# Performance work log

Measured on AMD Instinct MI355X. Metric: run time of the kernel, lower is better.

## Reference

```python
import jax, jax.numpy as jnp
import numpy as np

# Dimensions
F = 512      # features = len(in_degrees)
D = 64
S, B, N = 1, 64, 256   # outer sample dim, hyper-batch, points per batch element
C = 128      # conditioner (phi) feature dim
P = F * F + F  # flat params per batch element: weight + bias


def _mask():
    # hidden-layer MADE degrees: arange(F) % max(1, D-1) + min(1, D-1)
    d = jnp.arange(F) % (D - 1) + 1
    # MaskedLinear hidden mask: out_degrees[:, None] >= in_degrees[None, :]
    # (the torch code reshapes the square [F,F] mask, which is an identity
    #  memory reshape, so element (i, j) = (d[i] >= d[j]))
    return (d[:, None] >= d[None, :]).astype(jnp.float32)


def setup_inputs() -> dict:
    key = jax.random.key(0)
    k1, k2, k3, k4 = jax.random.split(key, 4)
    return {
        "inputs": jax.random.normal(k1, (S, B, N, F), jnp.float32),
        "phi": jax.random.normal(k2, (S, B, C), jnp.float32),
        "Wc": jax.random.normal(k3, (P, C), jnp.float32) * 0.02,
        "bc": jax.random.normal(k4, (P,), jnp.float32) * 0.02,
    }


def reference(inputs, phi, Wc, bc):
    # Conditioner net: linear hypernetwork phi -> flat per-batch params.
    params = jnp.einsum('sbc,pc->sbp', phi, Wc) + bc          # [S,B,P]
    w = params[..., : F * F].reshape(S, B, F, F)               # [S,B,F_in,F_out]
    b = params[..., F * F : F * F + F]                         # [S,B,F]
    mw = w * _mask()                                           # masked per-batch weights

    # Residual block (no batch norm, dropout p=0): act -> masked linear (x2) -> residual
    t = jax.nn.relu(inputs)
    t = jnp.einsum('sbni,sbik->sbnk', t, mw) + b[:, :, None, :]
    t = jax.nn.relu(t)
    # Both MaskedLinear layers split the SAME conditioner output, so they share
    # (w, b); only the masks could differ, and with these degrees they coincide.
    t = jnp.einsum('sbni,sbik->sbnk', t, mw) + b[:, :, None, :]
    return inputs + t
```

## Files before the change

### kernel.cpp

```cpp
#include <hip/hip_runtime.h>
#include <hip/hip_bf16.h>

#define F_   512
#define FF_  (512 * 512)
#define C_   128

typedef __attribute__((ext_vector_type(4))) float f32x4;
typedef __attribute__((ext_vector_type(8))) short s16x8;
typedef __attribute__((ext_vector_type(4))) unsigned short u16x4;

__device__ __forceinline__ unsigned short f2bf(float f) {
    union { __hip_bfloat16 h; unsigned short u; } c;
    c.h = __float2bfloat16(f);
    return c.u;
}

__device__ __forceinline__ s16x8 pack8(f32x4 lo, f32x4 hi) {
    s16x8 r;
    r[0] = (short)f2bf(lo[0]); r[1] = (short)f2bf(lo[1]);
    r[2] = (short)f2bf(lo[2]); r[3] = (short)f2bf(lo[3]);
    r[4] = (short)f2bf(hi[0]); r[5] = (short)f2bf(hi[1]);
    r[6] = (short)f2bf(hi[2]); r[7] = (short)f2bf(hi[3]);
    return r;
}

#define GLDS16(gp, lp)                                                         \
    __builtin_amdgcn_global_load_lds(                                          \
        (const __attribute__((address_space(1))) void*)(gp),                   \
        (__attribute__((address_space(3))) void*)(lp), 16, 0, 0)

__global__ __launch_bounds__(256) void k0_prepack(
    const float* __restrict__ phi, unsigned short* __restrict__ phiP)
{
    const int t = threadIdx.x;
#pragma unroll
    for (int j = 0; j < 4; ++j) {
        int e = (j << 8) + t;
        int lane = e & 63, mk = e >> 6;
        int m = mk >> 2, kk = mk & 3;
        int brow = lane & 15, quad = lane >> 4;
        const float* p = phi + ((m << 4) + brow) * C_ + kk * 32 + (quad << 3);
        s16x8 v = pack8(*(const f32x4*)p, *(const f32x4*)(p + 4));
        *(s16x8*)&phiP[e << 3] = v;
    }
}

__global__ __launch_bounds__(256, 2) void k1_params(
    const unsigned short* __restrict__ phiP, const float* __restrict__ Wc,
    const float* __restrict__ bc, unsigned short* __restrict__ wT,
    float* __restrict__ biasWS, const float* __restrict__ phi)
{
    const int blk = blockIdx.x;
    const int tid = threadIdx.x;

    if (blk >= 512) {
        int g = ((blk - 512) << 8) + tid;
        int k = g >> 6, b = g & 63;
        const f32x4* w4 = (const f32x4*)(Wc + (size_t)(FF_ + k) * C_);
        const f32x4* p4 = (const f32x4*)(phi + b * C_);
        float acc = bc[FF_ + k];
#pragma unroll
        for (int c = 0; c < 32; ++c) {
            f32x4 a = w4[c], q = p4[c];
            acc += a[0]*q[0] + a[1]*q[1] + a[2]*q[2] + a[3]*q[3];
        }
        biasWS[(b << 9) + k] = acc;
        return;
    }

    __shared__ __align__(16) char stg[4][2][8192];

    const int lane = tid & 63, wave = tid >> 6, quad = lane >> 4;
    const int w  = (blk << 2) + wave;
    const int i0 = (w & 31) << 4;
    const int k0 = (w >> 5) << 3;

    s16x8 bfrP[4][4];
#pragma unroll
    for (int mk = 0; mk < 16; ++mk)
        bfrP[mk >> 2][mk & 3] = *(const s16x8*)&phiP[((mk << 6) + lane) << 3];

    f32x4 biasv[4][2];
#pragma unroll
    for (int rr = 0; rr < 4; ++rr) {
        const float* p = bc + (i0 + (quad << 2) + rr) * F_ + k0;
        biasv[rr][0] = *(const f32x4*)p;
        biasv[rr][1] = *(const f32x4*)(p + 4);
    }

    unsigned keepm = 0;
    {
#pragma unroll
        for (int ct = 0; ct < 8; ++ct) {
            int dk = (k0 + ct) % 63;
#pragma unroll
            for (int rr = 0; rr < 4; ++rr) {
                int di = (i0 + (quad << 2) + rr) % 63;
                if (di >= dk) keepm |= 1u << ((ct << 2) + rr);
            }
        }
    }
    int maxd = i0 % 63 + 15; maxd = maxd > 62 ? 62 : maxd;
    unsigned skipm = 0;
#pragma unroll
    for (int ct = 0; ct < 8; ++ct)
        if (((k0 + ct) % 63) > maxd) skipm |= 1u << ct;

    const int r2 = lane >> 5, s = lane & 31;
    char* const stw0 = stg[wave][0];
    char* const stw1 = stg[wave][1];

    auto STAGE = [&](int ct, char* dst) {
        const bool sk = (skipm >> ct) & 1;
        const int  k  = k0 + ct;
#pragma unroll
        for (int j = 0; j < 8; ++j) {
            int row = (j << 1) + r2;
            int isrc = sk ? i0 : (i0 + row);
            const char* src = (const char*)(Wc + ((size_t)(isrc * F_ + k)) * C_)
                            + ((s << 4) ^ ((row & 7) << 6));
            GLDS16(src, dst + (row << 9) + ((s << 4) ^ ((row & 7) << 6)));
        }
    };

    asm volatile("s_waitcnt vmcnt(0)" ::: "memory");

    auto STAGE2 = [&](int ct, char* dst) {
        const bool sk = (skipm >> ct) & 1;
        const int  k  = k0 + ct;
#pragma unroll
        for (int j = 0; j < 8; ++j) {
            int row = (j << 1) + r2;
            int isrc = sk ? i0 : (i0 + row);
            const char* src = (const char*)(Wc + ((size_t)(isrc * F_ + k)) * C_)
                            + ((s << 4) ^ ((row & 7) << 6));
            GLDS16(src, dst + (j << 10));
        }
    };
    (void)STAGE;

    STAGE2(0, stw0);

#pragma unroll
    for (int ct = 0; ct < 8; ++ct) {
        char* bufc = (ct & 1) ? stw1 : stw0;
        if (ct < 7) STAGE2(ct + 1, (ct & 1) ? stw0 : stw1);

        if (ct == 0)      asm volatile("s_waitcnt vmcnt(8)"  ::: "memory");
        else if (ct < 7)  asm volatile("s_waitcnt vmcnt(12)" ::: "memory");
        else              asm volatile("s_waitcnt vmcnt(4)"  ::: "memory");
        __builtin_amdgcn_sched_barrier(0);

        f32x4 acc[4];
#pragma unroll
        for (int bt = 0; bt < 4; ++bt) acc[bt] = (f32x4){0.f, 0.f, 0.f, 0.f};

        const bool sk = (skipm >> ct) & 1;
        if (!sk) {
            const int rowB = (lane & 15) << 9;
            const int swz  = (lane & 7) << 6;
#pragma unroll
            for (int kk = 0; kk < 4; ++kk) {
                int x0 = ((kk << 7) + (quad << 5)) ^ swz;
                int x1 = ((kk << 7) + (quad << 5) + 16) ^ swz;
                f32x4 lo = *(const f32x4*)(bufc + rowB + x0);
                f32x4 hi = *(const f32x4*)(bufc + rowB + x1);
                s16x8 aW = pack8(lo, hi);
#pragma unroll
                for (int bt = 0; bt < 4; ++bt)
                    acc[bt] = __builtin_amdgcn_mfma_f32_16x16x32_bf16(
                        aW, bfrP[bt][kk], acc[bt], 0, 0, 0);
            }
        }

        const int k = k0 + ct;
#pragma unroll
        for (int bt = 0; bt < 4; ++bt) {
            u16x4 v;
#pragma unroll
            for (int rr = 0; rr < 4; ++rr) {
                bool kp = (!sk) && ((keepm >> ((ct << 2) + rr)) & 1);
                float bv = (ct < 4) ? biasv[rr][0][ct] : biasv[rr][1][ct - 4];
                v[rr] = kp ? f2bf(acc[bt][rr] + bv) : (unsigned short)0;
            }
            int b = (bt << 4) + (lane & 15);
            *(u16x4*)&wT[(((size_t)((b << 9) + k)) << 9) + i0 + (quad << 2)] = v;
        }
    }
}

#define SMEM_BOFF 66560
#define CHUNK_B   32768
#define SMEM_TOT  (66560 + 2 * 32768)

__global__ __launch_bounds__(512) void k2_apply(
    const float* __restrict__ X, const unsigned short* __restrict__ wT,
    const float* __restrict__ biasWS, float* __restrict__ out)
{
    extern __shared__ char smem[];
    unsigned short* A_lds = (unsigned short*)smem;

    const int blk = blockIdx.x;
    const int sw  = ((blk & 7) << 5) + (blk >> 3);
    const int b   = sw >> 2;
    const int n0  = (sw & 3) << 6;

    const int tid = threadIdx.x, lane = tid & 63, wave = tid >> 6;
    const int wn = wave >> 2, wk = wave & 3;

    const float* Xb = X + (((size_t)(b * 256 + n0)) << 9);
    float*       Ob = out + (((size_t)(b * 256 + n0)) << 9);
    const unsigned short* wTb = wT + ((size_t)b << 18);

    float biasr[8];
#pragma unroll
    for (int nt = 0; nt < 8; ++nt)
        biasr[nt] = biasWS[(b << 9) + (wk << 7) + (nt << 4) + (lane & 15)];

    {
        const f32x4* X4 = (const f32x4*)Xb;
#pragma unroll
        for (int j = 0; j < 16; ++j) {
            int f = (j << 9) + tid;
            int row = f >> 7, c4 = f & 127;
            f32x4 v = X4[f];
            u16x4 h;
#pragma unroll
            for (int e = 0; e < 4; ++e) h[e] = f2bf(fmaxf(v[e], 0.f));
            *(u16x4*)&A_lds[row * 520 + (c4 << 2)] = h;
        }
    }

    const int srcslot = ((lane & 3) ^ ((lane >> 3) & 3)) << 3;

    f32x4 acc[2][8];

    for (int phase = 0; phase < 2; ++phase) {
#pragma unroll
        for (int mt = 0; mt < 2; ++mt)
#pragma unroll
            for (int nt = 0; nt < 8; ++nt) acc[mt][nt] = (f32x4){0.f, 0.f, 0.f, 0.f};

#pragma unroll
        for (int g = 0; g < 4; ++g) {
            int krow = (wave << 6) + (g << 4) + (lane >> 2);
            const unsigned short* src = wTb + ((size_t)krow << 9) + srcslot;
            char* lp = smem + SMEM_BOFF + (((wave << 6) + (g << 4)) << 6);
            GLDS16(src, lp);
        }
        asm volatile("s_waitcnt vmcnt(0)" ::: "memory");
        __syncthreads();

        for (int c = 0; c < 16; ++c) {
            const int cur = c & 1;
            if (c < 15) {
                const int i0n = (c + 1) << 5;
#pragma unroll
                for (int g = 0; g < 4; ++g) {
                    int krow = (wave << 6) + (g << 4) + (lane >> 2);
                    const unsigned short* src = wTb + ((size_t)krow << 9) + i0n + srcslot;
                    char* lp = smem + SMEM_BOFF + (cur ^ 1) * CHUNK_B
                             + (((wave << 6) + (g << 4)) << 6);
                    GLDS16(src, lp);
                }
            }
            const int i0c = c << 5;
            s16x8 afr[2];
#pragma unroll
            for (int mt = 0; mt < 2; ++mt) {
                int n = (wn << 5) + (mt << 4) + (lane & 15);
                afr[mt] = *(const s16x8*)&A_lds[n * 520 + i0c + ((lane >> 4) << 3)];
            }
            const unsigned short* Bb =
                (const unsigned short*)(smem + SMEM_BOFF + cur * CHUNK_B);
#pragma unroll
            for (int nt = 0; nt < 8; ++nt) {
                int k = (wk << 7) + (nt << 4) + (lane & 15);
                int slot = (((lane >> 4) ^ ((k >> 1) & 3)) << 3);
                s16x8 bfr = *(const s16x8*)&Bb[(k << 5) + slot];
#pragma unroll
                for (int mt = 0; mt < 2; ++mt)
                    acc[mt][nt] = __builtin_amdgcn_mfma_f32_16x16x32_bf16(
                        afr[mt], bfr, acc[mt][nt], 0, 0, 0);
            }
            asm volatile("s_waitcnt vmcnt(0)" ::: "memory");
            __syncthreads();
        }

        if (phase == 0) {
#pragma unroll
            for (int mt = 0; mt < 2; ++mt)
#pragma unroll
                for (int nt = 0; nt < 8; ++nt) {
                    int k = (wk << 7) + (nt << 4) + (lane & 15);
#pragma unroll
                    for (int r = 0; r < 4; ++r) {
                        int n = (wn << 5) + (mt << 4) + ((lane >> 4) << 2) + r;
                        A_lds[n * 520 + k] =
                            f2bf(fmaxf(acc[mt][nt][r] + biasr[nt], 0.f));
                    }
                }
            __syncthreads();
        }
    }

#pragma unroll
    for (int mt = 0; mt < 2; ++mt)
#pragma unroll
        for (int nt = 0; nt < 8; ++nt) {
            int k = (wk << 7) + (nt << 4) + (lane & 15);
#pragma unroll
            for (int r = 0; r < 4; ++r) {
                int n = (wn << 5) + (mt << 4) + ((lane >> 4) << 2) + r;
                size_t off = ((size_t)n << 9) + k;
                Ob[off] = Xb[off] + acc[mt][nt][r] + biasr[nt];
            }
        }
}

extern "C" void kernel_launch(void* const* d_in, const int* in_sizes, int n_in,
                              void* d_out, int out_size, void* d_ws, size_t ws_size,
                              hipStream_t stream) {
    const float* inputs = (const float*)d_in[0];
    const float* phi    = (const float*)d_in[1];
    const float* Wc     = (const float*)d_in[2];
    const float* bc     = (const float*)d_in[3];
    float* out = (float*)d_out;

    unsigned short* wT = (unsigned short*)d_ws;
    float* biasWS = (float*)((char*)d_ws + (size_t)64 * 512 * 512 * 2);
    unsigned short* phiP =
        (unsigned short*)((char*)d_ws + (size_t)64 * 512 * 512 * 2 + 64 * 512 * 4);

    hipLaunchKernelGGL(k0_prepack, dim3(1), dim3(256), 0, stream, phi, phiP);

    hipLaunchKernelGGL(k1_params, dim3(640), dim3(256), 0, stream,
                       phiP, Wc, bc, wT, biasWS, phi);

    hipFuncSetAttribute((const void*)k2_apply,
                        hipFuncAttributeMaxDynamicSharedMemorySize, SMEM_TOT);
    hipLaunchKernelGGL(k2_apply, dim3(256), dim3(512), SMEM_TOT, stream,
                       inputs, wT, biasWS, out);
}
```

Baseline: 71.81 us.

## Halve k1 LDS staging buffers and raise occupancy with half-row pipeline

The params kernel now stages each Wc row tile in two 256-byte halves, which halves the per-wave LDS double buffer from 8 KB to 4 KB per stage. Launch bounds rise from 2 to 4 blocks per CU so more waves can hide global-load latency. The inner loop becomes 16 half-steps, accumulating over two halves before storing. The cost is finer-grained waits and tighter register limits, which could cause spills.

```diff
diff --git a/kernel.cpp b/kernel.cpp
--- a/kernel.cpp
+++ b/kernel.cpp
@@ -45,7 +45,7 @@
     }
 }
 
-__global__ __launch_bounds__(256, 2) void k1_params(
+__global__ __launch_bounds__(256, 4) void k1_params(
     const unsigned short* __restrict__ phiP, const float* __restrict__ Wc,
     const float* __restrict__ bc, unsigned short* __restrict__ wT,
     float* __restrict__ biasWS, const float* __restrict__ phi)
@@ -68,7 +68,7 @@
         return;
     }
 
-    __shared__ __align__(16) char stg[4][2][8192];
+    __shared__ __align__(16) char stg[4][2][4096];
 
     const int lane = tid & 63, wave = tid >> 6, quad = lane >> 4;
     const int w  = (blk << 2) + wave;
@@ -89,15 +89,13 @@
     }
 
     unsigned keepm = 0;
-    {
-#pragma unroll
-        for (int ct = 0; ct < 8; ++ct) {
-            int dk = (k0 + ct) % 63;
-#pragma unroll
-            for (int rr = 0; rr < 4; ++rr) {
-                int di = (i0 + (quad << 2) + rr) % 63;
-                if (di >= dk) keepm |= 1u << ((ct << 2) + rr);
-            }
+#pragma unroll
+    for (int ct = 0; ct < 8; ++ct) {
+        int dk = (k0 + ct) % 63;
+#pragma unroll
+        for (int rr = 0; rr < 4; ++rr) {
+            int di = (i0 + (quad << 2) + rr) % 63;
+            if (di >= dk) keepm |= 1u << ((ct << 2) + rr);
         }
     }
     int maxd = i0 % 63 + 15; maxd = maxd > 62 ? 62 : maxd;
@@ -106,85 +104,79 @@
     for (int ct = 0; ct < 8; ++ct)
         if (((k0 + ct) % 63) > maxd) skipm |= 1u << ct;
 
-    const int r2 = lane >> 5, s = lane & 31;
     char* const stw0 = stg[wave][0];
     char* const stw1 = stg[wave][1];
-
-    auto STAGE = [&](int ct, char* dst) {
+    const int lq = lane >> 4;
+
+    auto STAGE = [&](int h, char* dst) {
+        const int ct = h >> 1, half = h & 1;
         const bool sk = (skipm >> ct) & 1;
-        const int  k  = k0 + ct;
-#pragma unroll
-        for (int j = 0; j < 8; ++j) {
-            int row = (j << 1) + r2;
+        const int k = k0 + ct;
+#pragma unroll
+        for (int j = 0; j < 4; ++j) {
+            int row = (j << 2) + lq;
             int isrc = sk ? i0 : (i0 + row);
             const char* src = (const char*)(Wc + ((size_t)(isrc * F_ + k)) * C_)
-                            + ((s << 4) ^ ((row & 7) << 6));
-            GLDS16(src, dst + (row << 9) + ((s << 4) ^ ((row & 7) << 6)));
+                            + (half << 8)
+                            + ((((lane & 15) ^ (row & 7)) << 4));
+            GLDS16(src, dst + (j << 10));
         }
     };
 
-    asm volatile("s_waitcnt vmcnt(0)" ::: "memory");
-
-    auto STAGE2 = [&](int ct, char* dst) {
+    STAGE(0, stw0);
+
+    f32x4 acc[4];
+
+#pragma unroll
+    for (int h = 0; h < 16; ++h) {
+        if (h < 15) STAGE(h + 1, ((h + 1) & 1) ? stw1 : stw0);
+
+        if      (h == 0)  asm volatile("s_waitcnt vmcnt(4)" ::: "memory");
+        else if (h == 15) asm volatile("s_waitcnt vmcnt(0)" ::: "memory");
+        else if (h & 1)   asm volatile("s_waitcnt vmcnt(4)" ::: "memory");
+        else              asm volatile("s_waitcnt vmcnt(8)" ::: "memory");
+        __builtin_amdgcn_sched_barrier(0);
+
+        const int ct = h >> 1, half = h & 1;
         const bool sk = (skipm >> ct) & 1;
-        const int  k  = k0 + ct;
-#pragma unroll
-        for (int j = 0; j < 8; ++j) {
-            int row = (j << 1) + r2;
-            int isrc = sk ? i0 : (i0 + row);
-            const char* src = (const char*)(Wc + ((size_t)(isrc * F_ + k)) * C_)
-                            + ((s << 4) ^ ((row & 7) << 6));
-            GLDS16(src, dst + (j << 10));
-        }
-    };
-    (void)STAGE;
-
-    STAGE2(0, stw0);
-
-#pragma unroll
-    for (int ct = 0; ct < 8; ++ct) {
-        char* bufc = (ct & 1) ? stw1 : stw0;
-        if (ct < 7) STAGE2(ct + 1, (ct & 1) ? stw0 : stw1);
-
-        if (ct == 0)      asm volatile("s_waitcnt vmcnt(8)"  ::: "memory");
-        else if (ct < 7)  asm volatile("s_waitcnt vmcnt(12)" ::: "memory");
-        else              asm volatile("s_waitcnt vmcnt(4)"  ::: "memory");
-        __builtin_amdgcn_sched_barrier(0);
-
-        f32x4 acc[4];
-#pragma unroll
-        for (int bt = 0; bt < 4; ++bt) acc[bt] = (f32x4){0.f, 0.f, 0.f, 0.f};
-
-        const bool sk = (skipm >> ct) & 1;
+
+        if (half == 0)
+#pragma unroll
+            for (int bt = 0; bt < 4; ++bt) acc[bt] = (f32x4){0.f, 0.f, 0.f, 0.f};
+
         if (!sk) {
-            const int rowB = (lane & 15) << 9;
-            const int swz  = (lane & 7) << 6;
-#pragma unroll
-            for (int kk = 0; kk < 4; ++kk) {
-                int x0 = ((kk << 7) + (quad << 5)) ^ swz;
-                int x1 = ((kk << 7) + (quad << 5) + 16) ^ swz;
-                f32x4 lo = *(const f32x4*)(bufc + rowB + x0);
-                f32x4 hi = *(const f32x4*)(bufc + rowB + x1);
+            char* bufc = (h & 1) ? stw1 : stw0;
+            const int r = lane & 15;
+            const int rbase = r << 8;
+            const int rx = r & 7;
+#pragma unroll
+            for (int kl = 0; kl < 2; ++kl) {
+                int u0 = (kl << 3) + (quad << 1);
+                f32x4 lo = *(const f32x4*)(bufc + rbase + ((u0 ^ rx) << 4));
+                f32x4 hi = *(const f32x4*)(bufc + rbase + (((u0 + 1) ^ rx) << 4));
                 s16x8 aW = pack8(lo, hi);
+                const int kkg = (half << 1) + kl;
 #pragma unroll
                 for (int bt = 0; bt < 4; ++bt)
                     acc[bt] = __builtin_amdgcn_mfma_f32_16x16x32_bf16(
-                        aW, bfrP[bt][kk], acc[bt], 0, 0, 0);
-            }
-        }
-
-        const int k = k0 + ct;
-#pragma unroll
-        for (int bt = 0; bt < 4; ++bt) {
-            u16x4 v;
-#pragma unroll
-            for (int rr = 0; rr < 4; ++rr) {
-                bool kp = (!sk) && ((keepm >> ((ct << 2) + rr)) & 1);
-                float bv = (ct < 4) ? biasv[rr][0][ct] : biasv[rr][1][ct - 4];
-                v[rr] = kp ? f2bf(acc[bt][rr] + bv) : (unsigned short)0;
-            }
-            int b = (bt << 4) + (lane & 15);
-            *(u16x4*)&wT[(((size_t)((b << 9) + k)) << 9) + i0 + (quad << 2)] = v;
+                        aW, bfrP[bt][kkg], acc[bt], 0, 0, 0);
+            }
+        }
+
+        if (half == 1) {
+            const int k = k0 + ct;
+#pragma unroll
+            for (int bt = 0; bt < 4; ++bt) {
+                u16x4 v;
+#pragma unroll
+                for (int rr = 0; rr < 4; ++rr) {
+                    bool kp = (!sk) && ((keepm >> ((ct << 2) + rr)) & 1);
+                    float bv = (ct < 4) ? biasv[rr][0][ct] : biasv[rr][1][ct - 4];
+                    v[rr] = kp ? f2bf(acc[bt][rr] + bv) : (unsigned short)0;
+                }
+                int b = (bt << 4) + (lane & 15);
+                *(u16x4*)&wT[(((size_t)((b << 9) + k)) << 9) + i0 + (quad << 2)] = v;
+            }
         }
     }
 }
```

New measurement: 97.84 us. 1.36x slower.
